# Kernel tuning notes

Measured on AMD Instinct MI355X. Metric: run time of the kernel, lower is better.

The kernel has to match this reference:

```python
import jax, jax.numpy as jnp
import numpy as np

STRIDE = 2

def setup_inputs() -> dict:
    key = jax.random.key(0)
    k1, k2 = jax.random.split(key)
    x = jax.random.normal(k1, (32, 128, 112, 112), dtype=jnp.float32)
    # matches nn.init.normal_(std=0.1)
    weight = jax.random.normal(k2, (256, 128, 3, 3), dtype=jnp.float32) * 0.1
    return {"x": x, "weight": weight}

def reference(x, weight):
    # Equivalent to the tile-loop: valid cross-correlation, no bias, stride=STRIDE.
    # x: (B, Cin, H, W); weight: (Cout, Cin, k, k) -> (B, Cout, w, w)
    return jax.lax.conv_general_dilated(
        x, weight,
        window_strides=(STRIDE, STRIDE),
        padding="VALID",
        dimension_numbers=("NCHW", "OIHW", "NCHW"),
    )
```

## Files before the change

kernel.cpp:

```cpp
#include <hip/hip_runtime.h>


#define BATCH 32
#define CIN   128
#define H     112
#define W     112
#define COUT  256
#define OH    55
#define OW    55
#define NPIX  (OH*OW)
#define NTOT  (BATCH*NPIX)

typedef __bf16 bf16x8 __attribute__((ext_vector_type(8)));
typedef float  f32x4  __attribute__((ext_vector_type(4)));

__device__ __forceinline__ unsigned short f2bf(float f) {
    unsigned u = __float_as_uint(f);
    u += 0x7FFFu + ((u >> 16) & 1u);
    return (unsigned short)(u >> 16);
}

__device__ __forceinline__ void gld_lds16(const void* g, void* l) {
    __builtin_amdgcn_global_load_lds((__attribute__((address_space(1))) void*)g,
                                     (__attribute__((address_space(3))) void*)l,
                                     16, 0, 0);
}

__global__ __launch_bounds__(256) void relayout_w_k(const float* __restrict__ w,
                                                    unsigned short* __restrict__ wt) {
    int o = blockIdx.x * 256 + threadIdx.x;
    if (o >= 9 * COUT * CIN) return;
    int cin  = o & (CIN - 1);
    int r    = o >> 7;
    int cout = r & (COUT - 1);
    int tap  = r >> 8;
    wt[o] = f2bf(w[((size_t)cout * CIN + cin) * 9 + tap]);
}

__global__ __launch_bounds__(256) void relayout_x_k(const float* __restrict__ x,
                                                    unsigned short* __restrict__ xs) {
    __shared__ __align__(16) unsigned short tile[W * 130 + 2];
    const int bh = blockIdx.x;
    const int b  = bh / H;
    const int h  = bh - b * H;
    const float* xr = x + (size_t)b * CIN * (H * W) + (size_t)h * W;
    const int t = threadIdx.x;
    for (int e = t; e < CIN * W; e += 256) {
        int c = e / W;
        int w = e - c * W;
        tile[w * 130 + c] = f2bf(xr[(size_t)c * (H * W) + w]);
    }
    __syncthreads();
    unsigned int* dst = (unsigned int*)(xs + (size_t)bh * (W * CIN));
    const unsigned int* src = (const unsigned int*)tile;
    for (int e = t; e < (W * CIN) / 2; e += 256) {
        int w  = e >> 6;
        int c2 = e & 63;
        dst[e] = src[w * 65 + c2];
    }
}

__global__ __launch_bounds__(256) void conv_mfma_k(const unsigned short* __restrict__ xs,
                                                   const unsigned short* __restrict__ wt,
                                                   float* __restrict__ out) {
    __shared__ __align__(16) unsigned short Alds[128 * 32];
    __shared__ __align__(16) unsigned short Blds[128 * 32];

    const int t    = threadIdx.x;
    const int wave = t >> 6;
    const int lane = t & 63;
    const int m0   = blockIdx.y * 128;
    const int n0   = blockIdx.x * 128;

    const int srow = t >> 2;
    const int scol = (t & 3) * 8;
    unsigned short* ldsA = Alds + wave * 512;
    unsigned short* ldsB = Blds + wave * 512;

    int xb[2];
#pragma unroll
    for (int i = 0; i < 2; ++i) {
        int nn = n0 + srow + i * 64;
        if (nn >= NTOT) nn = NTOT - 1;
        int b  = nn / NPIX;
        int rp = nn - b * NPIX;
        int oh = rp / OW;
        int ow = rp - oh * OW;
        xb[i] = ((b * H + 2 * oh) * W + 2 * ow) * CIN;
    }

    const int lrow   = lane & 15;
    const int koff   = (lane >> 4) * 8;
    const int wave_m = (wave & 1) * 64;
    const int wave_n = (wave >> 1) * 64;

    f32x4 acc[4][4];
#pragma unroll
    for (int mi = 0; mi < 4; ++mi)
#pragma unroll
        for (int ni = 0; ni < 4; ++ni)
            acc[mi][ni] = (f32x4){0.f, 0.f, 0.f, 0.f};

    for (int tap = 0; tap < 9; ++tap) {
        const int r = tap / 3;
        const int s = tap - 3 * r;
        const int toff = (r * W + s) * CIN;
        const unsigned short* wtap = wt + tap * (COUT * CIN) + (m0 + srow) * CIN + scol;
        const unsigned short* xst  = xs + toff + scol;
#pragma unroll
        for (int kb = 0; kb < 4; ++kb) {
            const int cin0 = kb * 32;
            gld_lds16(wtap + cin0,            ldsA);
            gld_lds16(wtap + 64 * CIN + cin0, ldsA + 2048);
            gld_lds16(xst + xb[0] + cin0,     ldsB);
            gld_lds16(xst + xb[1] + cin0,     ldsB + 2048);
            __syncthreads();

            bf16x8 af[4], bfr[4];
#pragma unroll
            for (int mi = 0; mi < 4; ++mi)
                af[mi] = *(const bf16x8*)(Alds + (wave_m + mi * 16 + lrow) * 32 + koff);
#pragma unroll
            for (int ni = 0; ni < 4; ++ni)
                bfr[ni] = *(const bf16x8*)(Blds + (wave_n + ni * 16 + lrow) * 32 + koff);
#pragma unroll
            for (int mi = 0; mi < 4; ++mi)
#pragma unroll
                for (int ni = 0; ni < 4; ++ni)
                    acc[mi][ni] = __builtin_amdgcn_mfma_f32_16x16x32_bf16(af[mi], bfr[ni], acc[mi][ni], 0, 0, 0);
            __syncthreads();
        }
    }

    long obase[4];
    int  okn[4];
#pragma unroll
    for (int ni = 0; ni < 4; ++ni) {
        int nn = n0 + wave_n + ni * 16 + lrow;
        okn[ni] = (nn < NTOT);
        if (!okn[ni]) nn = 0;
        int b   = nn / NPIX;
        int pix = nn - b * NPIX;
        obase[ni] = (long)b * (COUT * NPIX) + pix;
    }
    const int mrow = (lane >> 4) * 4;
#pragma unroll
    for (int mi = 0; mi < 4; ++mi) {
#pragma unroll
        for (int rr = 0; rr < 4; ++rr) {
            int  m  = m0 + wave_m + mi * 16 + mrow + rr;
            long mo = (long)m * NPIX;
#pragma unroll
            for (int ni = 0; ni < 4; ++ni)
                if (okn[ni]) out[obase[ni] + mo] = acc[mi][ni][rr];
        }
    }
}

__global__ __launch_bounds__(256) void direct_k(const float* __restrict__ x,
                                                const float* __restrict__ w,
                                                float* __restrict__ out) {
    const int pix = blockIdx.x * 256 + threadIdx.x;
    if (pix >= NPIX) return;
    const int b = blockIdx.z, cout0 = blockIdx.y * 8;
    const int oh = pix / OW, ow = pix - oh * OW;
    float acc[8];
#pragma unroll
    for (int i = 0; i < 8; ++i) acc[i] = 0.f;
    const float* xbp = x + ((size_t)b * CIN) * (H * W) + (size_t)(oh * 2) * W + ow * 2;
    const float* wb  = w + (size_t)cout0 * (CIN * 9);
    for (int cin = 0; cin < CIN; ++cin) {
        const float* xp = xbp + (size_t)cin * (H * W);
        float xv[9];
#pragma unroll
        for (int r = 0; r < 3; ++r) {
            xv[r * 3 + 0] = xp[r * W + 0];
            xv[r * 3 + 1] = xp[r * W + 1];
            xv[r * 3 + 2] = xp[r * W + 2];
        }
#pragma unroll
        for (int c = 0; c < 8; ++c) {
            const float* wp = wb + (size_t)c * (CIN * 9) + cin * 9;
#pragma unroll
            for (int k = 0; k < 9; ++k) acc[c] = fmaf(wp[k], xv[k], acc[c]);
        }
    }
    const size_t ob = ((size_t)b * COUT + cout0) * NPIX + pix;
#pragma unroll
    for (int c = 0; c < 8; ++c) out[ob + (size_t)c * NPIX] = acc[c];
}

extern "C" void kernel_launch(void* const* d_in, const int* in_sizes, int n_in,
                              void* d_out, int out_size, void* d_ws, size_t ws_size,
                              hipStream_t stream) {
    const float* x = (const float*)d_in[0];
    const float* w = (const float*)d_in[1];
    float* out = (float*)d_out;

    const size_t xs_elems = (size_t)BATCH * H * W * CIN;
    const size_t wt_elems = (size_t)9 * COUT * CIN;
    const size_t need = (xs_elems + wt_elems) * 2;

    if (ws_size >= need) {
        unsigned short* xs = (unsigned short*)d_ws;
        unsigned short* wt = xs + xs_elems;
        relayout_w_k<<<(9 * COUT * CIN + 255) / 256, 256, 0, stream>>>(w, wt);
        relayout_x_k<<<BATCH * H, 256, 0, stream>>>(x, xs);
        dim3 grid((NTOT + 127) / 128, COUT / 128);
        conv_mfma_k<<<grid, dim3(256), 0, stream>>>(xs, wt, out);
    } else {
        dim3 grid((NPIX + 255) / 256, COUT / 8, BATCH);
        direct_k<<<grid, dim3(256), 0, stream>>>(x, w, out);
    }
}
```

Before: 422.6 us.

## Double-buffer LDS in conv GEMM and vectorize input relayout transpose

The MFMA conv main loop is flattened into 36 K-steps with two LDS buffers. The next step's global-to-LDS loads are issued right after a single barrier, so they can overlap the current step's MFMAs and the second barrier per step goes away. The input relayout kernel now reads float4 and writes uint4, with the shared tile padded to a row pitch of 136. The change risks the compiler inserting conservative waitcnts that serialize the async loads. The new tile pitch may also cause LDS bank conflicts on the strided transpose writes.

```diff
diff --git a/kernel.cpp b/kernel.cpp
--- a/kernel.cpp
+++ b/kernel.cpp
@@ -37,34 +37,43 @@
     wt[o] = f2bf(w[((size_t)cout * CIN + cin) * 9 + tap]);
 }
 
+#define XP 136
 __global__ __launch_bounds__(256) void relayout_x_k(const float* __restrict__ x,
                                                     unsigned short* __restrict__ xs) {
-    __shared__ __align__(16) unsigned short tile[W * 130 + 2];
+    __shared__ __align__(16) unsigned short tile[W * XP];
     const int bh = blockIdx.x;
     const int b  = bh / H;
     const int h  = bh - b * H;
     const float* xr = x + (size_t)b * CIN * (H * W) + (size_t)h * W;
     const int t = threadIdx.x;
-    for (int e = t; e < CIN * W; e += 256) {
-        int c = e / W;
-        int w = e - c * W;
-        tile[w * 130 + c] = f2bf(xr[(size_t)c * (H * W) + w]);
+#pragma unroll
+    for (int i = 0; i < 14; ++i) {
+        int e  = t + i * 256;
+        int c  = e / 28;
+        int w4 = e - c * 28;
+        float4 v = *(const float4*)(xr + (size_t)c * (H * W) + w4 * 4);
+        int base = (w4 * 4) * XP + c;
+        tile[base]          = f2bf(v.x);
+        tile[base + XP]     = f2bf(v.y);
+        tile[base + 2 * XP] = f2bf(v.z);
+        tile[base + 3 * XP] = f2bf(v.w);
     }
     __syncthreads();
-    unsigned int* dst = (unsigned int*)(xs + (size_t)bh * (W * CIN));
-    const unsigned int* src = (const unsigned int*)tile;
-    for (int e = t; e < (W * CIN) / 2; e += 256) {
-        int w  = e >> 6;
-        int c2 = e & 63;
-        dst[e] = src[w * 65 + c2];
+    uint4* dst = (uint4*)(xs + (size_t)bh * (W * CIN));
+#pragma unroll
+    for (int i = 0; i < 7; ++i) {
+        int e  = t + i * 256;
+        int w  = e >> 4;
+        int c8 = e & 15;
+        dst[e] = *(const uint4*)(tile + w * XP + c8 * 8);
     }
 }
 
 __global__ __launch_bounds__(256) void conv_mfma_k(const unsigned short* __restrict__ xs,
                                                    const unsigned short* __restrict__ wt,
                                                    float* __restrict__ out) {
-    __shared__ __align__(16) unsigned short Alds[128 * 32];
-    __shared__ __align__(16) unsigned short Blds[128 * 32];
+    __shared__ __align__(16) unsigned short Alds[2][128 * 32];
+    __shared__ __align__(16) unsigned short Blds[2][128 * 32];
 
     const int t    = threadIdx.x;
     const int wave = t >> 6;
@@ -74,8 +83,6 @@
 
     const int srow = t >> 2;
     const int scol = (t & 3) * 8;
-    unsigned short* ldsA = Alds + wave * 512;
-    unsigned short* ldsB = Blds + wave * 512;
 
     int xb[2];
 #pragma unroll
@@ -101,35 +108,41 @@
         for (int ni = 0; ni < 4; ++ni)
             acc[mi][ni] = (f32x4){0.f, 0.f, 0.f, 0.f};
 
-    for (int tap = 0; tap < 9; ++tap) {
-        const int r = tap / 3;
-        const int s = tap - 3 * r;
-        const int toff = (r * W + s) * CIN;
-        const unsigned short* wtap = wt + tap * (COUT * CIN) + (m0 + srow) * CIN + scol;
-        const unsigned short* xst  = xs + toff + scol;
-#pragma unroll
-        for (int kb = 0; kb < 4; ++kb) {
-            const int cin0 = kb * 32;
-            gld_lds16(wtap + cin0,            ldsA);
-            gld_lds16(wtap + 64 * CIN + cin0, ldsA + 2048);
-            gld_lds16(xst + xb[0] + cin0,     ldsB);
-            gld_lds16(xst + xb[1] + cin0,     ldsB + 2048);
-            __syncthreads();
-
-            bf16x8 af[4], bfr[4];
-#pragma unroll
-            for (int mi = 0; mi < 4; ++mi)
-                af[mi] = *(const bf16x8*)(Alds + (wave_m + mi * 16 + lrow) * 32 + koff);
+    auto issue = [&](int ks, int buf) {
+        int tap  = ks >> 2;
+        int cin0 = (ks & 3) * 32;
+        int r    = (tap >= 6) ? 2 : (tap >= 3) ? 1 : 0;
+        int s    = tap - 3 * r;
+        int toff = (r * W + s) * CIN;
+        const unsigned short* wtap = wt + tap * (COUT * CIN) + (m0 + srow) * CIN + scol + cin0;
+        const unsigned short* xst  = xs + toff + scol + cin0;
+        unsigned short* la = &Alds[buf][0] + wave * 512;
+        unsigned short* lb = &Blds[buf][0] + wave * 512;
+        gld_lds16(wtap,             la);
+        gld_lds16(wtap + 64 * CIN,  la + 2048);
+        gld_lds16(xst + xb[0],      lb);
+        gld_lds16(xst + xb[1],      lb + 2048);
+    };
+
+    issue(0, 0);
+#pragma unroll 2
+    for (int ks = 0; ks < 36; ++ks) {
+        const int buf = ks & 1;
+        __syncthreads();
+        if (ks + 1 < 36) issue(ks + 1, buf ^ 1);
+
+        bf16x8 af[4], bfr[4];
+#pragma unroll
+        for (int mi = 0; mi < 4; ++mi)
+            af[mi] = *(const bf16x8*)(&Alds[buf][0] + (wave_m + mi * 16 + lrow) * 32 + koff);
+#pragma unroll
+        for (int ni = 0; ni < 4; ++ni)
+            bfr[ni] = *(const bf16x8*)(&Blds[buf][0] + (wave_n + ni * 16 + lrow) * 32 + koff);
+#pragma unroll
+        for (int mi = 0; mi < 4; ++mi)
 #pragma unroll
             for (int ni = 0; ni < 4; ++ni)
-                bfr[ni] = *(const bf16x8*)(Blds + (wave_n + ni * 16 + lrow) * 32 + koff);
-#pragma unroll
-            for (int mi = 0; mi < 4; ++mi)
-#pragma unroll
-                for (int ni = 0; ni < 4; ++ni)
-                    acc[mi][ni] = __builtin_amdgcn_mfma_f32_16x16x32_bf16(af[mi], bfr[ni], acc[mi][ni], 0, 0, 0);
-            __syncthreads();
-        }
+                acc[mi][ni] = __builtin_amdgcn_mfma_f32_16x16x32_bf16(af[mi], bfr[ni], acc[mi][ni], 0, 0, 0);
     }
 
     long obase[4];
```

Result: faster. 410.2 us (-3.0%).
